# Optimization experiments

Hardware: AMD Instinct MI355X
Metric: run time of the kernel (lower is better)

Reference implementation:

```python
import jax, jax.numpy as jnp
import numpy as np

B, C, H, W = 4, 96, 64, 64
NLAYERS, DSTATE, EXPAND, DCONV = 2, 16, 2, 4
DIN = EXPAND * C          # 192
DTRANK = (C + 15) // 16   # 6
EPS = 1e-5


def setup_inputs() -> dict:
    key = jax.random.key(0)
    ks = jax.random.split(key, 10)
    s = jnp.float32(0.02)
    f32 = jnp.float32
    inp = {
        "x": jax.random.normal(ks[0], (B, C, H, W), f32),
        "ln_g": jnp.ones((NLAYERS, C), f32),
        "ln_b": jnp.zeros((NLAYERS, C), f32),
        "in_w": jax.random.normal(ks[1], (NLAYERS, C, 2 * DIN), f32) * s,
        "conv_w": jax.random.normal(ks[2], (NLAYERS, DIN, DCONV), f32) * s,
        "conv_b": jnp.zeros((NLAYERS, DIN), f32),
        "xproj_w": jax.random.normal(ks[3], (NLAYERS, DIN, DTRANK + 2 * DSTATE), f32) * s,
        "dt_w": jax.random.normal(ks[4], (NLAYERS, DTRANK, DIN), f32) * s,
        "dt_b": jnp.full((NLAYERS, DIN), -4.6, f32),  # softplus(-4.6) ~ 0.01
        "A_log": jnp.log(jnp.tile(jnp.arange(1, DSTATE + 1, dtype=f32)[None, None, :], (NLAYERS, DIN, 1))),
        "Dp": jnp.ones((NLAYERS, DIN), f32),
        "out_w": jax.random.normal(ks[5], (NLAYERS, DIN, C), f32) * s,
        "gp_w": jax.random.normal(ks[6], (C, C), f32) * s,
        "gp_b": jnp.zeros((C,), f32),
        "fus_w": jax.random.normal(ks[7], (C, 2 * C), f32) * s,
        "fus_b": jnp.zeros((C,), f32),
        "bn_g": jnp.ones((C,), f32),
        "bn_b": jnp.zeros((C,), f32),
    }
    return inp


def _mamba_block(seq, ln_g, ln_b, in_w, conv_w, conv_b, xproj_w, dt_w, dt_b, A_log, Dp, out_w):
    # seq: (B, L, C)
    L = seq.shape[1]
    mu = seq.mean(-1, keepdims=True)
    var = ((seq - mu) ** 2).mean(-1, keepdims=True)
    h = (seq - mu) * jax.lax.rsqrt(var + EPS) * ln_g + ln_b
    xz = h @ in_w                                   # (B, L, 2*DIN)
    xs, z = jnp.split(xz, 2, axis=-1)
    # causal depthwise conv1d along L (kernel DCONV)
    xp = jnp.pad(xs, ((0, 0), (DCONV - 1, 0), (0, 0)))
    xc = sum(conv_w[:, k] * xp[:, k:k + L, :] for k in range(DCONV)) + conv_b
    xc = jax.nn.silu(xc)
    dbl = xc @ xproj_w                              # (B, L, DTRANK+2*DSTATE)
    dt = dbl[..., :DTRANK]
    Bm = dbl[..., DTRANK:DTRANK + DSTATE]
    Cm = dbl[..., DTRANK + DSTATE:]
    delta = jax.nn.softplus(dt @ dt_w + dt_b)       # (B, L, DIN)
    A = -jnp.exp(A_log)                             # (DIN, DSTATE)
    dA = jnp.exp(delta[..., None] * A)              # (B, L, DIN, DSTATE)
    dBx = delta[..., None] * Bm[:, :, None, :] * xc[..., None]
    def comb(a, b):  # compose linear recurrences h -> A*h + u
        return (a[0] * b[0], b[0] * a[1] + b[1])
    hstates = jax.lax.associative_scan(comb, (dA, dBx), axis=1)[1]
    y = jnp.einsum('blds,bls->bld', hstates, Cm) + Dp * xc
    y = y * jax.nn.silu(z)
    return y @ out_w


def _forward(x, ln_g, ln_b, in_w, conv_w, conv_b, xproj_w, dt_w, dt_b, A_log, Dp, out_w,
             gp_w, gp_b, fus_w, fus_b, bn_g, bn_b):
    b, c, h, w = x.shape
    L = h * w
    residual = x
    seq = x.reshape(b, c, L).transpose(0, 2, 1)     # (B, L, C)
    for i in range(NLAYERS):
        seq = seq + _mamba_block(seq, ln_g[i], ln_b[i], in_w[i], conv_w[i], conv_b[i],
                                 xproj_w[i], dt_w[i], dt_b[i], A_log[i], Dp[i], out_w[i])
    mamba_out = seq.transpose(0, 2, 1).reshape(b, c, h, w)
    # global pool -> 1x1 conv -> relu -> bilinear upsample of 1x1 == broadcast
    gp = jax.nn.relu(x.mean((2, 3)) @ gp_w.T + gp_b)          # (B, C)
    gfull = jnp.broadcast_to(gp[:, :, None, None], (b, c, h, w))
    cat = jnp.concatenate([mamba_out, gfull], axis=1)         # (B, 2C, H, W)
    out = jnp.einsum('oc,bchw->bohw', fus_w, cat) + fus_b[None, :, None, None]
    # BatchNorm2d (training-mode batch statistics)
    mu = out.mean((0, 2, 3))
    var = out.var((0, 2, 3))
    out = (out - mu[None, :, None, None]) * jax.lax.rsqrt(var + EPS)[None, :, None, None]
    out = out * bn_g[None, :, None, None] + bn_b[None, :, None, None]
    return out + residual


def reference(x, ln_g, ln_b, in_w, conv_w, conv_b, xproj_w, dt_w, dt_b, A_log, Dp, out_w,
              gp_w, gp_b, fus_w, fus_b, bn_g, bn_b):
    return _forward(x, ln_g, ln_b, in_w, conv_w, conv_b, xproj_w, dt_w, dt_b, A_log, Dp, out_w,
                    gp_w, gp_b, fus_w, fus_b, bn_g, bn_b)
```

## Files before the change

### kernel.cpp

```cpp
#include <hip/hip_runtime.h>
#include <math.h>

#define BB 4
#define C 96
#define LL 4096
#define DIN 192
#define DS 16
#define DT 6
#define DX 38
#define NCHAIN (BB*DIN*DS)
#define NBLK_FUSE 512
#define EPSF 1e-5f

__device__ __forceinline__ float silu_f(float x){ return x / (1.0f + __expf(-x)); }
__device__ __forceinline__ float softplus_f(float x){ return x > 20.0f ? x : log1pf(__expf(x)); }

__global__ void k_transpose_in(const float* __restrict__ x, float* __restrict__ seq){
    __shared__ float t[32][33];
    int b = blockIdx.z;
    int l0 = blockIdx.x*32, c0 = blockIdx.y*32;
    int tx = threadIdx.x, ty = threadIdx.y;
    t[ty][tx] = x[((size_t)b*C + c0 + ty)*LL + l0 + tx];
    __syncthreads();
    seq[((size_t)b*LL + l0 + ty)*C + c0 + tx] = t[tx][ty];
}

__global__ void k_xmean(const float* __restrict__ x, float* __restrict__ xmean){
    __shared__ float red[256];
    int bc = blockIdx.x;
    const float* p = x + (size_t)bc*LL;
    float s = 0.f;
    for (int i = threadIdx.x; i < LL; i += 256) s += p[i];
    red[threadIdx.x] = s; __syncthreads();
    for (int o = 128; o; o >>= 1){
        if (threadIdx.x < o) red[threadIdx.x] += red[threadIdx.x+o];
        __syncthreads();
    }
    if (threadIdx.x == 0) xmean[bc] = red[0] * (1.f/LL);
}

__global__ void k_prep_fusw(const float* __restrict__ fus_w, float* __restrict__ fus_wt){
    int idx = blockIdx.x*256 + threadIdx.x;
    if (idx < C*C){
        int c = idx / C, o = idx % C;
        fus_wt[idx] = fus_w[(size_t)o*(2*C) + c];
    }
}

__global__ __launch_bounds__(512) void k_ln_inproj(const float* __restrict__ seq,
        const float* __restrict__ ln_g, const float* __restrict__ ln_b,
        const float* __restrict__ in_w, float* __restrict__ xz){
    __shared__ float hb[32][C];
    int tid = threadIdx.x;
    int wave = tid >> 6, lane = tid & 63;
    int t0 = blockIdx.x*32;
    int tw = wave*4;
    #pragma unroll
    for (int tt = 0; tt < 4; tt++){
        int tl = tw + tt;
        const float* row = seq + (size_t)(t0 + tl)*C;
        float v0 = row[lane];
        float v1 = (lane < 32) ? row[64 + lane] : 0.f;
        float sum = v0 + v1;
        for (int off = 32; off; off >>= 1) sum += __shfl_xor(sum, off);
        float mu = sum * (1.f/C);
        float d0 = v0 - mu;
        float d1 = (lane < 32) ? (v1 - mu) : 0.f;
        float sq = d0*d0 + d1*d1;
        for (int off = 32; off; off >>= 1) sq += __shfl_xor(sq, off);
        float rstd = rsqrtf(sq * (1.f/C) + EPSF);
        hb[tl][lane] = d0*rstd*ln_g[lane] + ln_b[lane];
        if (lane < 32) hb[tl][64+lane] = d1*rstd*ln_g[64+lane] + ln_b[64+lane];
    }
    __syncthreads();
    float acc[4][6];
    #pragma unroll
    for (int t = 0; t < 4; t++)
        #pragma unroll
        for (int j = 0; j < 6; j++) acc[t][j] = 0.f;
    for (int c = 0; c < C; c++){
        const float* wr = in_w + (size_t)c*(2*DIN);
        float w0 = wr[lane], w1 = wr[lane+64], w2 = wr[lane+128],
              w3 = wr[lane+192], w4 = wr[lane+256], w5 = wr[lane+320];
        #pragma unroll
        for (int t = 0; t < 4; t++){
            float hv = hb[tw + t][c];
            acc[t][0] = fmaf(hv, w0, acc[t][0]);
            acc[t][1] = fmaf(hv, w1, acc[t][1]);
            acc[t][2] = fmaf(hv, w2, acc[t][2]);
            acc[t][3] = fmaf(hv, w3, acc[t][3]);
            acc[t][4] = fmaf(hv, w4, acc[t][4]);
            acc[t][5] = fmaf(hv, w5, acc[t][5]);
        }
    }
    #pragma unroll
    for (int t = 0; t < 4; t++){
        float* o = xz + (size_t)(t0 + tw + t)*(2*DIN);
        #pragma unroll
        for (int j = 0; j < 6; j++) o[lane + 64*j] = acc[t][j];
    }
}

__global__ __launch_bounds__(768) void k_conv_xproj(const float* __restrict__ xz,
        const float* __restrict__ conv_w, const float* __restrict__ conv_b,
        const float* __restrict__ xproj_w, const float* __restrict__ dt_w,
        const float* __restrict__ dt_b,
        float* __restrict__ xc, float* __restrict__ delta,
        float* __restrict__ Bm, float* __restrict__ Cm){
    __shared__ float xcb[32][DIN+1];
    __shared__ float dbl[32][DX];
    int tid = threadIdx.x;
    int t0 = blockIdx.x*32;
    int l0 = t0 & (LL - 1);
    {
        int d   = tid % DIN;
        int seg = tid / DIN;
        int tseg = t0 + seg*8;
        const float* cw = conv_w + d*4;
        float c0 = cw[0], c1 = cw[1], c2 = cw[2], c3 = cw[3];
        float bias = conv_b[d];
        float x0 = 0.f, x1 = 0.f, x2 = 0.f;
        if (seg > 0 || l0 > 0){
            x0 = xz[((size_t)(tseg-3))*(2*DIN) + d];
            x1 = xz[((size_t)(tseg-2))*(2*DIN) + d];
            x2 = xz[((size_t)(tseg-1))*(2*DIN) + d];
        }
        float xv[8];
        #pragma unroll
        for (int j = 0; j < 8; j++)
            xv[j] = xz[((size_t)(tseg + j))*(2*DIN) + d];
        #pragma unroll
        for (int j = 0; j < 8; j++){
            float a = fmaf(c3, xv[j], fmaf(c2, x2, fmaf(c1, x1, fmaf(c0, x0, bias))));
            float s = silu_f(a);
            xcb[seg*8 + j][d] = s;
            xc[((size_t)(tseg + j))*DIN + d] = s;
            x0 = x1; x1 = x2; x2 = xv[j];
        }
    }
    __syncthreads();
    for (int idx = tid; idx < 32*DX; idx += 768){
        int tl = idx / DX, o = idx % DX;
        const float* wo = xproj_w + o;
        float a0 = 0.f, a1 = 0.f;
        for (int c = 0; c < DIN; c += 2){
            a0 = fmaf(xcb[tl][c],   wo[(size_t)c*DX],     a0);
            a1 = fmaf(xcb[tl][c+1], wo[(size_t)(c+1)*DX], a1);
        }
        float a = a0 + a1;
        dbl[tl][o] = a;
        int tg = t0 + tl;
        if (o >= DT && o < DT+DS)      Bm[(size_t)tg*DS + (o-DT)] = a;
        else if (o >= DT+DS)           Cm[(size_t)tg*DS + (o-DT-DS)] = a;
    }
    __syncthreads();
    for (int idx = tid; idx < 32*DIN; idx += 768){
        int tl = idx / DIN, d = idx % DIN;
        float a = dt_b[d];
        #pragma unroll
        for (int r = 0; r < DT; r++) a = fmaf(dbl[tl][r], dt_w[r*DIN + d], a);
        delta[(size_t)(t0 + tl)*DIN + d] = softplus_f(a);
    }
}

template<int NCHT>
__global__ __launch_bounds__(384) void k_scan_A(const float* __restrict__ delta,
        const float* __restrict__ xc, const float* __restrict__ Bm,
        const float* __restrict__ A_log,
        float* __restrict__ Pbuf, float* __restrict__ Sbuf){
    const int CLT = LL / NCHT;
    int tid = threadIdx.x;
    int d = tid >> 1, half = tid & 1;
    int ch = blockIdx.x % NCHT;
    int b  = blockIdx.x / NCHT;
    const float4* ap = (const float4*)(A_log + (size_t)d*DS + half*8);
    float4 a0 = ap[0], a1 = ap[1];
    float Av[8] = {a0.x,a0.y,a0.z,a0.w, a1.x,a1.y,a1.z,a1.w};
    float P[8], hs[8];
    #pragma unroll
    for (int s = 0; s < 8; s++){ Av[s] = -__expf(Av[s]); P[s] = 1.f; hs[s] = 0.f; }
    size_t tbase = (size_t)b*LL + (size_t)ch*CLT;
    const float*  dp = delta + tbase*DIN + d;
    const float*  xp = xc    + tbase*DIN + d;
    const float4* bp = (const float4*)(Bm + tbase*DS + half*8);
    for (int i = 0; i < CLT; i++){
        float dv = dp[(size_t)i*DIN];
        float xv = xp[(size_t)i*DIN];
        float4 b0 = bp[4*i], b1 = bp[4*i+1];
        float bb[8] = {b0.x,b0.y,b0.z,b0.w, b1.x,b1.y,b1.z,b1.w};
        float dxv = dv*xv;
        #pragma unroll
        for (int s = 0; s < 8; s++){
            float dA = __expf(dv*Av[s]);
            hs[s] = fmaf(dA, hs[s], bb[s]*dxv);
            P[s] *= dA;
        }
    }
    size_t base = (size_t)ch*NCHAIN + ((size_t)b*DIN + d)*DS + half*8;
    float4* Pb = (float4*)(Pbuf + base);
    float4* Sb = (float4*)(Sbuf + base);
    Pb[0] = make_float4(P[0],P[1],P[2],P[3]);
    Pb[1] = make_float4(P[4],P[5],P[6],P[7]);
    Sb[0] = make_float4(hs[0],hs[1],hs[2],hs[3]);
    Sb[1] = make_float4(hs[4],hs[5],hs[6],hs[7]);
}

template<int NCHT>
__global__ void k_scan_B(const float* __restrict__ Pbuf, float* __restrict__ Sbuf){
    int chain = blockIdx.x*256 + threadIdx.x;
    float h = 0.f;
    for (int ch = 0; ch < NCHT; ch++){
        size_t idx = (size_t)ch*NCHAIN + chain;
        float P = Pbuf[idx];
        float S = Sbuf[idx];
        Sbuf[idx] = h;
        h = fmaf(P, h, S);
    }
}

template<int NCHT>
__global__ __launch_bounds__(384) void k_scan_C(const float* __restrict__ delta,
        const float* __restrict__ xc, const float* __restrict__ Bm,
        const float* __restrict__ Cm,
        const float* __restrict__ A_log, const float* __restrict__ Dp,
        const float* __restrict__ Sbuf, float* __restrict__ yraw){
    const int CLT = LL / NCHT;
    int tid = threadIdx.x;
    int d = tid >> 1, half = tid & 1;
    int ch = blockIdx.x % NCHT;
    int b  = blockIdx.x / NCHT;
    const float4* ap = (const float4*)(A_log + (size_t)d*DS + half*8);
    float4 a0 = ap[0], a1 = ap[1];
    float Av[8] = {a0.x,a0.y,a0.z,a0.w, a1.x,a1.y,a1.z,a1.w};
    #pragma unroll
    for (int s = 0; s < 8; s++) Av[s] = -__expf(Av[s]);
    float Dv = Dp[d];
    size_t base = (size_t)ch*NCHAIN + ((size_t)b*DIN + d)*DS + half*8;
    const float4* Sb = (const float4*)(Sbuf + base);
    float4 h0 = Sb[0], h1 = Sb[1];
    float h[8] = {h0.x,h0.y,h0.z,h0.w, h1.x,h1.y,h1.z,h1.w};
    size_t tbase = (size_t)b*LL + (size_t)ch*CLT;
    const float*  dp = delta + tbase*DIN + d;
    const float*  xp = xc    + tbase*DIN + d;
    const float4* bp = (const float4*)(Bm + tbase*DS + half*8);
    const float4* cp = (const float4*)(Cm + tbase*DS + half*8);
    float* yp = yraw + tbase*DIN + d;
    for (int i = 0; i < CLT; i++){
        float dv = dp[(size_t)i*DIN];
        float xv = xp[(size_t)i*DIN];
        float4 b0 = bp[4*i], b1 = bp[4*i+1];
        float4 c0 = cp[4*i], c1 = cp[4*i+1];
        float bb[8] = {b0.x,b0.y,b0.z,b0.w, b1.x,b1.y,b1.z,b1.w};
        float cc[8] = {c0.x,c0.y,c0.z,c0.w, c1.x,c1.y,c1.z,c1.w};
        float dxv = dv*xv;
        float acc0 = 0.f, acc1 = 0.f;
        #pragma unroll
        for (int s = 0; s < 8; s += 2){
            float dA0 = __expf(dv*Av[s]);
            float dA1 = __expf(dv*Av[s+1]);
            h[s]   = fmaf(dA0, h[s],   bb[s]*dxv);
            h[s+1] = fmaf(dA1, h[s+1], bb[s+1]*dxv);
            acc0 = fmaf(h[s],   cc[s],   acc0);
            acc1 = fmaf(h[s+1], cc[s+1], acc1);
        }
        float contrib = acc0 + acc1;
        if (half == 0) contrib += Dv*xv;
        contrib += __shfl_xor(contrib, 1);
        if (half == 0) yp[(size_t)i*DIN] = contrib;
    }
}

__global__ __launch_bounds__(512) void k_outproj(const float* __restrict__ yraw,
        const float* __restrict__ xz, const float* __restrict__ out_w,
        float* __restrict__ seq){
    __shared__ float ygb[32][DIN];
    int tid = threadIdx.x;
    int wave = tid >> 6, lane = tid & 63;
    int t0 = blockIdx.x*32;
    for (int idx = tid; idx < 32*DIN; idx += 512){
        int tl = idx / DIN, d = idx % DIN;
        int t = t0 + tl;
        float yv = yraw[(size_t)t*DIN + d];
        float zv = xz[(size_t)t*(2*DIN) + DIN + d];
        ygb[tl][d] = yv * silu_f(zv);
    }
    __syncthreads();
    float a0[4], a1[4];
    #pragma unroll
    for (int t = 0; t < 4; t++){ a0[t] = 0.f; a1[t] = 0.f; }
    int tw = wave*4;
    for (int d = 0; d < DIN; d++){
        const float* wr = out_w + (size_t)d*C;
        float w0 = wr[lane];
        float w1 = (lane < 32) ? wr[64 + lane] : 0.f;
        #pragma unroll
        for (int t = 0; t < 4; t++){
            float yv = ygb[tw + t][d];
            a0[t] = fmaf(yv, w0, a0[t]);
            a1[t] = fmaf(yv, w1, a1[t]);
        }
    }
    #pragma unroll
    for (int t = 0; t < 4; t++){
        size_t tg = (size_t)(t0 + tw + t);
        seq[tg*C + lane] += a0[t];
        if (lane < 32) seq[tg*C + 64 + lane] += a1[t];
    }
}

__global__ void k_gp(const float* __restrict__ xmean, const float* __restrict__ gp_w,
        const float* __restrict__ gp_b, const float* __restrict__ fus_w,
        const float* __restrict__ fus_b, float* __restrict__ gconst){
    __shared__ float gp[BB*C];
    int tid = threadIdx.x;
    int b = tid / C, i = tid % C;
    float a = gp_b[i];
    for (int c = 0; c < C; c++) a = fmaf(xmean[b*C + c], gp_w[i*C + c], a);
    gp[tid] = fmaxf(a, 0.f);
    __syncthreads();
    float g = fus_b[i];
    for (int c = 0; c < C; c++) g = fmaf(fus_w[i*(2*C) + C + c], gp[b*C + c], g);
    gconst[tid] = g;
}

__global__ __launch_bounds__(256) void k_fuse(const float* __restrict__ seq,
        const float* __restrict__ fus_wt, const float* __restrict__ gconst,
        float* __restrict__ outpre, float* __restrict__ psum, float* __restrict__ psq){
    __shared__ float sb[32][C];
    __shared__ float bs[4][C], bq[4][C];
    int tid = threadIdx.x;
    int wave = tid >> 6, lane = tid & 63;
    int t0 = blockIdx.x*32;
    int b = t0 >> 12;
    for (int idx = tid; idx < 32*C; idx += 256){
        int tl = idx / C, c = idx % C;
        sb[tl][c] = seq[(size_t)(t0 + tl)*C + c];
    }
    __syncthreads();
    float g0 = gconst[b*C + lane];
    float g1 = (lane < 32) ? gconst[b*C + 64 + lane] : 0.f;
    float a0[8], a1[8];
    #pragma unroll
    for (int t = 0; t < 8; t++){ a0[t] = g0; a1[t] = g1; }
    int tw = wave*8;
    for (int c = 0; c < C; c++){
        const float* wr = fus_wt + (size_t)c*C;
        float w0 = wr[lane];
        float w1 = (lane < 32) ? wr[64 + lane] : 0.f;
        #pragma unroll
        for (int t = 0; t < 8; t++){
            float sv = sb[tw + t][c];
            a0[t] = fmaf(sv, w0, a0[t]);
            a1[t] = fmaf(sv, w1, a1[t]);
        }
    }
    float s0 = 0.f, q0 = 0.f, s1 = 0.f, q1 = 0.f;
    #pragma unroll
    for (int t = 0; t < 8; t++){
        size_t tg = (size_t)(t0 + tw + t);
        outpre[tg*C + lane] = a0[t];
        s0 += a0[t]; q0 += a0[t]*a0[t];
        if (lane < 32){
            outpre[tg*C + 64 + lane] = a1[t];
            s1 += a1[t]; q1 += a1[t]*a1[t];
        }
    }
    bs[wave][lane] = s0; bq[wave][lane] = q0;
    if (lane < 32){ bs[wave][64+lane] = s1; bq[wave][64+lane] = q1; }
    __syncthreads();
    if (tid < C){
        float s = 0.f, q = 0.f;
        #pragma unroll
        for (int w = 0; w < 4; w++){ s += bs[w][tid]; q += bq[w][tid]; }
        psum[(size_t)blockIdx.x*C + tid] = s;
        psq [(size_t)blockIdx.x*C + tid] = q;
    }
}

__global__ void k_bnstat(const float* __restrict__ psum, const float* __restrict__ psq,
        const float* __restrict__ bn_g, const float* __restrict__ bn_b,
        float* __restrict__ scale, float* __restrict__ shift){
    __shared__ float r1[256], r2[256];
    int o = blockIdx.x;
    float s1 = 0.f, s2 = 0.f;
    for (int i = threadIdx.x; i < NBLK_FUSE; i += 256){
        s1 += psum[(size_t)i*C + o];
        s2 += psq [(size_t)i*C + o];
    }
    r1[threadIdx.x] = s1; r2[threadIdx.x] = s2; __syncthreads();
    for (int off = 128; off; off >>= 1){
        if (threadIdx.x < off){ r1[threadIdx.x] += r1[threadIdx.x+off]; r2[threadIdx.x] += r2[threadIdx.x+off]; }
        __syncthreads();
    }
    if (threadIdx.x == 0){
        float N = (float)(BB*LL);
        float mu = r1[0] / N;
        float var = r2[0] / N - mu*mu;
        float sc = bn_g[o] * rsqrtf(var + EPSF);
        scale[o] = sc;
        shift[o] = bn_b[o] - mu*sc;
    }
}

__global__ void k_final(const float* __restrict__ outpre, const float* __restrict__ x,
        const float* __restrict__ scale, const float* __restrict__ shift,
        float* __restrict__ out){
    __shared__ float tle[32][33];
    int b = blockIdx.z;
    int l0 = blockIdx.x*32, o0 = blockIdx.y*32;
    int tx = threadIdx.x, ty = threadIdx.y;
    tle[ty][tx] = outpre[((size_t)b*LL + l0 + ty)*C + o0 + tx];
    __syncthreads();
    int o = o0 + ty;
    size_t idx = ((size_t)b*C + o)*LL + l0 + tx;
    out[idx] = tle[tx][ty]*scale[o] + shift[o] + x[idx];
}

extern "C" void kernel_launch(void* const* d_in, const int* in_sizes, int n_in,
                              void* d_out, int out_size, void* d_ws, size_t ws_size,
                              hipStream_t stream){
    const float* x      = (const float*)d_in[0];
    const float* ln_g   = (const float*)d_in[1];
    const float* ln_b   = (const float*)d_in[2];
    const float* in_w   = (const float*)d_in[3];
    const float* conv_w = (const float*)d_in[4];
    const float* conv_b = (const float*)d_in[5];
    const float* xproj_w= (const float*)d_in[6];
    const float* dt_w   = (const float*)d_in[7];
    const float* dt_b   = (const float*)d_in[8];
    const float* A_log  = (const float*)d_in[9];
    const float* Dp     = (const float*)d_in[10];
    const float* out_w  = (const float*)d_in[11];
    const float* gp_w   = (const float*)d_in[12];
    const float* gp_b   = (const float*)d_in[13];
    const float* fus_w  = (const float*)d_in[14];
    const float* fus_b  = (const float*)d_in[15];
    const float* bn_g   = (const float*)d_in[16];
    const float* bn_b   = (const float*)d_in[17];

    const size_t base_f = (size_t)BB*LL*C + (size_t)BB*LL*2*DIN + (size_t)BB*LL*DIN
                        + (size_t)BB*LL*DIN + (size_t)BB*LL*DS + (size_t)BB*LL*DS;
    const size_t small_f = BB*C + BB*C + C + C + (size_t)C*C;
    const size_t need256 = (base_f + 2*(size_t)256*NCHAIN + small_f) * sizeof(float);
    const int nch = (ws_size >= need256) ? 256 : 128;

    float* ws    = (float*)d_ws;
    float* seq   = ws;
    float* xz    = seq   + (size_t)BB*LL*C;
    float* xcb   = xz    + (size_t)BB*LL*2*DIN;
    float* delta = xcb   + (size_t)BB*LL*DIN;
    float* Bmb   = delta + (size_t)BB*LL*DIN;
    float* Cmb   = Bmb   + (size_t)BB*LL*DS;
    float* Pbuf  = Cmb   + (size_t)BB*LL*DS;
    float* Sbuf  = Pbuf  + (size_t)nch*NCHAIN;
    float* xmean = Sbuf  + (size_t)nch*NCHAIN;
    float* gconst= xmean + BB*C;
    float* scale = gconst+ BB*C;
    float* shift = scale + C;
    float* fus_wt= shift + C;
    float* yraw  = delta;
    float* outpre= xz;
    float* psum  = xz + (size_t)BB*LL*C;
    float* psq   = psum + (size_t)NBLK_FUSE*C;

    k_transpose_in<<<dim3(LL/32, C/32, BB), dim3(32,32), 0, stream>>>(x, seq);
    k_xmean<<<BB*C, 256, 0, stream>>>(x, xmean);
    k_prep_fusw<<<(C*C + 255)/256, 256, 0, stream>>>(fus_w, fus_wt);

    for (int layer = 0; layer < 2; layer++){
        const float* lng = ln_g   + (size_t)layer*C;
        const float* lnb = ln_b   + (size_t)layer*C;
        const float* inw = in_w   + (size_t)layer*C*2*DIN;
        const float* cw  = conv_w + (size_t)layer*DIN*4;
        const float* cb  = conv_b + (size_t)layer*DIN;
        const float* xpw = xproj_w+ (size_t)layer*DIN*DX;
        const float* dtw = dt_w   + (size_t)layer*DT*DIN;
        const float* dtb = dt_b   + (size_t)layer*DIN;
        const float* alog= A_log  + (size_t)layer*DIN*DS;
        const float* dpp = Dp     + (size_t)layer*DIN;
        const float* ow  = out_w  + (size_t)layer*DIN*C;

        k_ln_inproj <<<(BB*LL)/32, 512, 0, stream>>>(seq, lng, lnb, inw, xz);
        k_conv_xproj<<<(BB*LL)/32, 768, 0, stream>>>(xz, cw, cb, xpw, dtw, dtb, xcb, delta, Bmb, Cmb);
        if (nch == 256){
            k_scan_A<256><<<BB*256, 384, 0, stream>>>(delta, xcb, Bmb, alog, Pbuf, Sbuf);
            k_scan_B<256><<<NCHAIN/256, 256, 0, stream>>>(Pbuf, Sbuf);
            k_scan_C<256><<<BB*256, 384, 0, stream>>>(delta, xcb, Bmb, Cmb, alog, dpp, Sbuf, yraw);
        } else {
            k_scan_A<128><<<BB*128, 384, 0, stream>>>(delta, xcb, Bmb, alog, Pbuf, Sbuf);
            k_scan_B<128><<<NCHAIN/256, 256, 0, stream>>>(Pbuf, Sbuf);
            k_scan_C<128><<<BB*128, 384, 0, stream>>>(delta, xcb, Bmb, Cmb, alog, dpp, Sbuf, yraw);
        }
        k_outproj<<<(BB*LL)/32, 512, 0, stream>>>(yraw, xz, ow, seq);
    }

    k_gp<<<1, BB*C, 0, stream>>>(xmean, gp_w, gp_b, fus_w, fus_b, gconst);
    k_fuse<<<(BB*LL)/32, 256, 0, stream>>>(seq, fus_wt, gconst, outpre, psum, psq);
    k_bnstat<<<C, 256, 0, stream>>>(psum, psq, bn_g, bn_b, scale, shift);
    k_final<<<dim3(LL/32, C/32, BB), dim3(32,32), 0, stream>>>(outpre, x, scale, shift, (float*)d_out);
}
```

Measured before the change: 342.3 us.

## Fuse layernorm/in-projection with conv and x-projection, recomputing halo rows

Merges the layernorm plus in-projection kernel and the conv plus x-projection kernel into a single kernel. Each block recomputes three halo rows for the causal conv, so the xs half stays in LDS and is never written to global memory; only the z half goes to a smaller buffer. This removes a launch and a large global round trip of the xz tensor. The price is about 9% redundant in-projection work, five rows per wave with a wasted padded row, and lower parallelism in the conv stage (512 threads instead of 768).

```diff
diff --git a/kernel.cpp b/kernel.cpp
--- a/kernel.cpp
+++ b/kernel.cpp
@@ -47,118 +47,126 @@
     }
 }
 
-__global__ __launch_bounds__(512) void k_ln_inproj(const float* __restrict__ seq,
+#define XSB_OFF 0
+#define HB_OFF  6720
+#define XCB_OFF 6720
+#define DBL_OFF 0
+#define FRONT_LDS 12896
+
+__global__ __launch_bounds__(512) void k_front(const float* __restrict__ seq,
         const float* __restrict__ ln_g, const float* __restrict__ ln_b,
-        const float* __restrict__ in_w, float* __restrict__ xz){
-    __shared__ float hb[32][C];
+        const float* __restrict__ in_w,
+        const float* __restrict__ conv_w, const float* __restrict__ conv_b,
+        const float* __restrict__ xproj_w, const float* __restrict__ dt_w,
+        const float* __restrict__ dt_b,
+        float* __restrict__ zbuf, float* __restrict__ xc,
+        float* __restrict__ delta, float* __restrict__ Bm, float* __restrict__ Cm){
+    __shared__ float buf[FRONT_LDS];
+    float* xsb = buf + XSB_OFF;
+    float* hb  = buf + HB_OFF;
+    float* xcb = buf + XCB_OFF;
+    float* dbl = buf + DBL_OFF;
     int tid = threadIdx.x;
     int wave = tid >> 6, lane = tid & 63;
     int t0 = blockIdx.x*32;
-    int tw = wave*4;
-    #pragma unroll
-    for (int tt = 0; tt < 4; tt++){
-        int tl = tw + tt;
-        const float* row = seq + (size_t)(t0 + tl)*C;
-        float v0 = row[lane];
-        float v1 = (lane < 32) ? row[64 + lane] : 0.f;
-        float sum = v0 + v1;
-        for (int off = 32; off; off >>= 1) sum += __shfl_xor(sum, off);
-        float mu = sum * (1.f/C);
-        float d0 = v0 - mu;
-        float d1 = (lane < 32) ? (v1 - mu) : 0.f;
-        float sq = d0*d0 + d1*d1;
-        for (int off = 32; off; off >>= 1) sq += __shfl_xor(sq, off);
-        float rstd = rsqrtf(sq * (1.f/C) + EPSF);
-        hb[tl][lane] = d0*rstd*ln_g[lane] + ln_b[lane];
-        if (lane < 32) hb[tl][64+lane] = d1*rstd*ln_g[64+lane] + ln_b[64+lane];
-    }
-    __syncthreads();
-    float acc[4][6];
-    #pragma unroll
-    for (int t = 0; t < 4; t++)
-        #pragma unroll
-        for (int j = 0; j < 6; j++) acc[t][j] = 0.f;
+    int l0 = t0 & (LL - 1);
+    for (int r = wave; r < 35; r += 8){
+        bool valid = (l0 > 0) || (r >= 3);
+        float h0 = 0.f, h1 = 0.f;
+        if (valid){
+            const float* row = seq + (size_t)(t0 - 3 + r)*C;
+            float v0 = row[lane];
+            float v1 = (lane < 32) ? row[64 + lane] : 0.f;
+            float sum = v0 + v1;
+            for (int off = 32; off; off >>= 1) sum += __shfl_xor(sum, off);
+            float mu = sum * (1.f/C);
+            float d0 = v0 - mu;
+            float d1 = (lane < 32) ? (v1 - mu) : 0.f;
+            float sq = d0*d0 + d1*d1;
+            for (int off = 32; off; off >>= 1) sq += __shfl_xor(sq, off);
+            float rstd = rsqrtf(sq * (1.f/C) + EPSF);
+            h0 = d0*rstd*ln_g[lane] + ln_b[lane];
+            if (lane < 32) h1 = d1*rstd*ln_g[64+lane] + ln_b[64+lane];
+        }
+        hb[r*C + lane] = h0;
+        if (lane < 32) hb[r*C + 64 + lane] = h1;
+    }
+    __syncthreads();
+    int rows[5];
+    #pragma unroll
+    for (int k = 0; k < 5; k++){
+        int r = wave + 8*k;
+        rows[k] = (r < 35) ? r : 34;
+    }
+    float acc[5][6];
+    #pragma unroll
+    for (int k = 0; k < 5; k++)
+        #pragma unroll
+        for (int j = 0; j < 6; j++) acc[k][j] = 0.f;
     for (int c = 0; c < C; c++){
         const float* wr = in_w + (size_t)c*(2*DIN);
         float w0 = wr[lane], w1 = wr[lane+64], w2 = wr[lane+128],
               w3 = wr[lane+192], w4 = wr[lane+256], w5 = wr[lane+320];
         #pragma unroll
-        for (int t = 0; t < 4; t++){
-            float hv = hb[tw + t][c];
-            acc[t][0] = fmaf(hv, w0, acc[t][0]);
-            acc[t][1] = fmaf(hv, w1, acc[t][1]);
-            acc[t][2] = fmaf(hv, w2, acc[t][2]);
-            acc[t][3] = fmaf(hv, w3, acc[t][3]);
-            acc[t][4] = fmaf(hv, w4, acc[t][4]);
-            acc[t][5] = fmaf(hv, w5, acc[t][5]);
-        }
-    }
-    #pragma unroll
-    for (int t = 0; t < 4; t++){
-        float* o = xz + (size_t)(t0 + tw + t)*(2*DIN);
-        #pragma unroll
-        for (int j = 0; j < 6; j++) o[lane + 64*j] = acc[t][j];
-    }
-}
-
-__global__ __launch_bounds__(768) void k_conv_xproj(const float* __restrict__ xz,
-        const float* __restrict__ conv_w, const float* __restrict__ conv_b,
-        const float* __restrict__ xproj_w, const float* __restrict__ dt_w,
-        const float* __restrict__ dt_b,
-        float* __restrict__ xc, float* __restrict__ delta,
-        float* __restrict__ Bm, float* __restrict__ Cm){
-    __shared__ float xcb[32][DIN+1];
-    __shared__ float dbl[32][DX];
-    int tid = threadIdx.x;
-    int t0 = blockIdx.x*32;
-    int l0 = t0 & (LL - 1);
-    {
-        int d   = tid % DIN;
-        int seg = tid / DIN;
-        int tseg = t0 + seg*8;
+        for (int k = 0; k < 5; k++){
+            float hv = hb[rows[k]*C + c];
+            acc[k][0] = fmaf(hv, w0, acc[k][0]);
+            acc[k][1] = fmaf(hv, w1, acc[k][1]);
+            acc[k][2] = fmaf(hv, w2, acc[k][2]);
+            acc[k][3] = fmaf(hv, w3, acc[k][3]);
+            acc[k][4] = fmaf(hv, w4, acc[k][4]);
+            acc[k][5] = fmaf(hv, w5, acc[k][5]);
+        }
+    }
+    #pragma unroll
+    for (int k = 0; k < 5; k++){
+        int r = wave + 8*k;
+        if (r < 35){
+            xsb[r*DIN + lane]       = acc[k][0];
+            xsb[r*DIN + 64 + lane]  = acc[k][1];
+            xsb[r*DIN + 128 + lane] = acc[k][2];
+            if (r >= 3){
+                float* zp = zbuf + (size_t)(t0 + r - 3)*DIN;
+                zp[lane]       = acc[k][3];
+                zp[64 + lane]  = acc[k][4];
+                zp[128 + lane] = acc[k][5];
+            }
+        }
+    }
+    __syncthreads();
+    for (int idx = tid; idx < 32*DIN; idx += 512){
+        int tl = idx / DIN, d = idx % DIN;
         const float* cw = conv_w + d*4;
-        float c0 = cw[0], c1 = cw[1], c2 = cw[2], c3 = cw[3];
-        float bias = conv_b[d];
-        float x0 = 0.f, x1 = 0.f, x2 = 0.f;
-        if (seg > 0 || l0 > 0){
-            x0 = xz[((size_t)(tseg-3))*(2*DIN) + d];
-            x1 = xz[((size_t)(tseg-2))*(2*DIN) + d];
-            x2 = xz[((size_t)(tseg-1))*(2*DIN) + d];
-        }
-        float xv[8];
-        #pragma unroll
-        for (int j = 0; j < 8; j++)
-            xv[j] = xz[((size_t)(tseg + j))*(2*DIN) + d];
-        #pragma unroll
-        for (int j = 0; j < 8; j++){
-            float a = fmaf(c3, xv[j], fmaf(c2, x2, fmaf(c1, x1, fmaf(c0, x0, bias))));
-            float s = silu_f(a);
-            xcb[seg*8 + j][d] = s;
-            xc[((size_t)(tseg + j))*DIN + d] = s;
-            x0 = x1; x1 = x2; x2 = xv[j];
-        }
-    }
-    __syncthreads();
-    for (int idx = tid; idx < 32*DX; idx += 768){
+        float a = conv_b[d];
+        a = fmaf(cw[0], xsb[(tl+0)*DIN + d], a);
+        a = fmaf(cw[1], xsb[(tl+1)*DIN + d], a);
+        a = fmaf(cw[2], xsb[(tl+2)*DIN + d], a);
+        a = fmaf(cw[3], xsb[(tl+3)*DIN + d], a);
+        float s = silu_f(a);
+        xcb[tl*(DIN+1) + d] = s;
+        xc[(size_t)(t0 + tl)*DIN + d] = s;
+    }
+    __syncthreads();
+    for (int idx = tid; idx < 32*DX; idx += 512){
         int tl = idx / DX, o = idx % DX;
         const float* wo = xproj_w + o;
         float a0 = 0.f, a1 = 0.f;
         for (int c = 0; c < DIN; c += 2){
-            a0 = fmaf(xcb[tl][c],   wo[(size_t)c*DX],     a0);
-            a1 = fmaf(xcb[tl][c+1], wo[(size_t)(c+1)*DX], a1);
+            a0 = fmaf(xcb[tl*(DIN+1) + c],   wo[(size_t)c*DX],     a0);
+            a1 = fmaf(xcb[tl*(DIN+1) + c+1], wo[(size_t)(c+1)*DX], a1);
         }
         float a = a0 + a1;
-        dbl[tl][o] = a;
+        dbl[tl*DX + o] = a;
         int tg = t0 + tl;
         if (o >= DT && o < DT+DS)      Bm[(size_t)tg*DS + (o-DT)] = a;
         else if (o >= DT+DS)           Cm[(size_t)tg*DS + (o-DT-DS)] = a;
     }
     __syncthreads();
-    for (int idx = tid; idx < 32*DIN; idx += 768){
+    for (int idx = tid; idx < 32*DIN; idx += 512){
         int tl = idx / DIN, d = idx % DIN;
         float a = dt_b[d];
         #pragma unroll
-        for (int r = 0; r < DT; r++) a = fmaf(dbl[tl][r], dt_w[r*DIN + d], a);
+        for (int r = 0; r < DT; r++) a = fmaf(dbl[tl*DX + r], dt_w[r*DIN + d], a);
         delta[(size_t)(t0 + tl)*DIN + d] = softplus_f(a);
     }
 }
@@ -271,7 +279,7 @@
 }
 
 __global__ __launch_bounds__(512) void k_outproj(const float* __restrict__ yraw,
-        const float* __restrict__ xz, const float* __restrict__ out_w,
+        const float* __restrict__ zbuf, const float* __restrict__ out_w,
         float* __restrict__ seq){
     __shared__ float ygb[32][DIN];
     int tid = threadIdx.x;
@@ -281,7 +289,7 @@
         int tl = idx / DIN, d = idx % DIN;
         int t = t0 + tl;
         float yv = yraw[(size_t)t*DIN + d];
-        float zv = xz[(size_t)t*(2*DIN) + DIN + d];
+        float zv = zbuf[(size_t)t*DIN + d];
         ygb[tl][d] = yv * silu_f(zv);
     }
     __syncthreads();
@@ -438,17 +446,20 @@
     const float* bn_g   = (const float*)d_in[16];
     const float* bn_b   = (const float*)d_in[17];
 
-    const size_t base_f = (size_t)BB*LL*C + (size_t)BB*LL*2*DIN + (size_t)BB*LL*DIN
-                        + (size_t)BB*LL*DIN + (size_t)BB*LL*DS + (size_t)BB*LL*DS;
+    const size_t base_f = (size_t)BB*LL*C
+                        + (size_t)BB*LL*DIN
+                        + (size_t)BB*LL*DIN
+                        + (size_t)BB*LL*DIN
+                        + (size_t)BB*LL*DS + (size_t)BB*LL*DS;
     const size_t small_f = BB*C + BB*C + C + C + (size_t)C*C;
     const size_t need256 = (base_f + 2*(size_t)256*NCHAIN + small_f) * sizeof(float);
     const int nch = (ws_size >= need256) ? 256 : 128;
 
     float* ws    = (float*)d_ws;
     float* seq   = ws;
-    float* xz    = seq   + (size_t)BB*LL*C;
-    float* xcb   = xz    + (size_t)BB*LL*2*DIN;
-    float* delta = xcb   + (size_t)BB*LL*DIN;
+    float* zbuf  = seq   + (size_t)BB*LL*C;
+    float* xcbuf = zbuf  + (size_t)BB*LL*DIN;
+    float* delta = xcbuf + (size_t)BB*LL*DIN;
     float* Bmb   = delta + (size_t)BB*LL*DIN;
     float* Cmb   = Bmb   + (size_t)BB*LL*DS;
     float* Pbuf  = Cmb   + (size_t)BB*LL*DS;
@@ -459,8 +470,8 @@
     float* shift = scale + C;
     float* fus_wt= shift + C;
     float* yraw  = delta;
-    float* outpre= xz;
-    float* psum  = xz + (size_t)BB*LL*C;
+    float* outpre= zbuf;
+    float* psum  = zbuf + (size_t)BB*LL*C;
     float* psq   = psum + (size_t)NBLK_FUSE*C;
 
     k_transpose_in<<<dim3(LL/32, C/32, BB), dim3(32,32), 0, stream>>>(x, seq);
@@ -480,18 +491,18 @@
         const float* dpp = Dp     + (size_t)layer*DIN;
         const float* ow  = out_w  + (size_t)layer*DIN*C;
 
-        k_ln_inproj <<<(BB*LL)/32, 512, 0, stream>>>(seq, lng, lnb, inw, xz);
-        k_conv_xproj<<<(BB*LL)/32, 768, 0, stream>>>(xz, cw, cb, xpw, dtw, dtb, xcb, delta, Bmb, Cmb);
+        k_front<<<(BB*LL)/32, 512, 0, stream>>>(seq, lng, lnb, inw, cw, cb,
+                                                xpw, dtw, dtb, zbuf, xcbuf, delta, Bmb, Cmb);
         if (nch == 256){
-            k_scan_A<256><<<BB*256, 384, 0, stream>>>(delta, xcb, Bmb, alog, Pbuf, Sbuf);
+            k_scan_A<256><<<BB*256, 384, 0, stream>>>(delta, xcbuf, Bmb, alog, Pbuf, Sbuf);
             k_scan_B<256><<<NCHAIN/256, 256, 0, stream>>>(Pbuf, Sbuf);
-            k_scan_C<256><<<BB*256, 384, 0, stream>>>(delta, xcb, Bmb, Cmb, alog, dpp, Sbuf, yraw);
+            k_scan_C<256><<<BB*256, 384, 0, stream>>>(delta, xcbuf, Bmb, Cmb, alog, dpp, Sbuf, yraw);
         } else {
-            k_scan_A<128><<<BB*128, 384, 0, stream>>>(delta, xcb, Bmb, alog, Pbuf, Sbuf);
+            k_scan_A<128><<<BB*128, 384, 0, stream>>>(delta, xcbuf, Bmb, alog, Pbuf, Sbuf);
             k_scan_B<128><<<NCHAIN/256, 256, 0, stream>>>(Pbuf, Sbuf);
-            k_scan_C<128><<<BB*128, 384, 0, stream>>>(delta, xcb, Bmb, Cmb, alog, dpp, Sbuf, yraw);
-        }
-        k_outproj<<<(BB*LL)/32, 512, 0, stream>>>(yraw, xz, ow, seq);
+            k_scan_C<128><<<BB*128, 384, 0, stream>>>(delta, xcbuf, Bmb, Cmb, alog, dpp, Sbuf, yraw);
+        }
+        k_outproj<<<(BB*LL)/32, 512, 0, stream>>>(yraw, zbuf, ow, seq);
     }
 
     k_gp<<<1, BB*C, 0, stream>>>(xmean, gp_w, gp_b, fus_w, fus_b, gconst);
```

New measurement: 333.9 us. -2.4%, faster.
